# Optimization experiments

Hardware: AMD Instinct MI355X
Metric: run time of the kernel (lower is better)

Reference implementation:

```python
import jax, jax.numpy as jnp
import numpy as np

B, T, I, H, OUT, L = 256, 1200, 16, 128, 1, 2


def _lstm_layer(x, W_ih, W_hh, b_ih, b_hh):
    # x: [B, T, Din]; W_ih: [4H, Din]; W_hh: [4H, H]
    # Precompute input contribution for all timesteps (one big GEMM),
    # then scan only the recurrent part.
    pre = jnp.einsum('btd,gd->btg', x, W_ih) + b_ih + b_hh  # [B, T, 4H]
    pre = jnp.swapaxes(pre, 0, 1)  # [T, B, 4H]
    h0 = jnp.zeros((x.shape[0], W_hh.shape[1]), dtype=x.dtype)
    c0 = jnp.zeros_like(h0)

    def step(carry, p_t):
        h, c = carry
        g = p_t + h @ W_hh.T  # [B, 4H]
        i, f, gg, o = jnp.split(g, 4, axis=-1)  # torch gate order: i, f, g, o
        i = jax.nn.sigmoid(i)
        f = jax.nn.sigmoid(f)
        gg = jnp.tanh(gg)
        o = jax.nn.sigmoid(o)
        c = f * c + i * gg
        h = o * jnp.tanh(c)
        return (h, c), h

    (_, _), hs = jax.lax.scan(step, (h0, c0), pre)  # hs: [T, B, H]
    return jnp.swapaxes(hs, 0, 1)  # [B, T, H]


def setup_inputs() -> dict:
    key = jax.random.key(0)
    ks = jax.random.split(key, 12)
    s = 0.08  # small init scale to keep gates unsaturated
    inp = {
        'x': jax.random.normal(ks[0], (B, T, I), dtype=jnp.float32),
        'W_ih0': jax.random.normal(ks[1], (4 * H, I), dtype=jnp.float32) * s,
        'W_hh0': jax.random.normal(ks[2], (4 * H, H), dtype=jnp.float32) * s,
        'b_ih0': jax.random.normal(ks[3], (4 * H,), dtype=jnp.float32) * s,
        'b_hh0': jax.random.normal(ks[4], (4 * H,), dtype=jnp.float32) * s,
        'W_ih1': jax.random.normal(ks[5], (4 * H, H), dtype=jnp.float32) * s,
        'W_hh1': jax.random.normal(ks[6], (4 * H, H), dtype=jnp.float32) * s,
        'b_ih1': jax.random.normal(ks[7], (4 * H,), dtype=jnp.float32) * s,
        'b_hh1': jax.random.normal(ks[8], (4 * H,), dtype=jnp.float32) * s,
        'W_lin': jax.random.normal(ks[9], (OUT, H), dtype=jnp.float32) * s,
        'b_lin': jax.random.normal(ks[10], (OUT,), dtype=jnp.float32) * s,
    }
    return inp


def reference(x, W_ih0, W_hh0, b_ih0, b_hh0, W_ih1, W_hh1, b_ih1, b_hh1, W_lin, b_lin):
    h1 = _lstm_layer(x, W_ih0, W_hh0, b_ih0, b_hh0)   # [B, T, H]
    h2 = _lstm_layer(h1, W_ih1, W_hh1, b_ih1, b_hh1)  # [B, T, H]
    out = jax.nn.relu(h2)
    out = jnp.einsum('bth,oh->bto', out, W_lin) + b_lin  # [B, T, OUT]
    return out.reshape(-1, 12)  # [B*T*OUT/12, 12]
```

## Files before the change

### kernel.cpp

```cpp
#include <hip/hip_runtime.h>
#include <hip/hip_fp16.h>

#define B_ 256
#define T_ 1200
#define I_ 16
#define H_ 128
#define G4_ (4 * H_)

typedef __attribute__((ext_vector_type(2))) _Float16 h2;
typedef __attribute__((ext_vector_type(8))) _Float16 f16x8;

union f16x8u { f16x8 v; h2 h[4]; _Float16 s[8]; };

#if __has_builtin(__builtin_amdgcn_fdot2)
__device__ __forceinline__ float fdot2(h2 a, h2 b, float c) {
  return __builtin_amdgcn_fdot2(a, b, c, false);
}
#else
__device__ __forceinline__ float fdot2(h2 a, h2 b, float c) {
  return fmaf((float)a.x, (float)b.x, fmaf((float)a.y, (float)b.y, c));
}
#endif

template <int PAT>
__device__ __forceinline__ float qbcast(float x) {
  return __int_as_float(__builtin_amdgcn_update_dpp(0, __float_as_int(x), PAT, 0xF, 0xF, true));
}

__device__ __forceinline__ float wred(float x) {
  x += __int_as_float(__builtin_amdgcn_update_dpp(0, __float_as_int(x), 0x141, 0xF, 0xF, true));
  x += __int_as_float(__builtin_amdgcn_update_dpp(0, __float_as_int(x), 0x140, 0xF, 0xF, true));
  x += __shfl_xor(x, 16);
  x += __shfl_xor(x, 32);
  return x;
}

__device__ __forceinline__ float sigm(float x) {
  return __builtin_amdgcn_rcpf(1.f + __expf(-x));
}
__device__ __forceinline__ float tanh_(float x) {
  return 1.f - 2.f * __builtin_amdgcn_rcpf(1.f + __expf(2.f * x));
}

__device__ __forceinline__ void load_row_h2(const float* __restrict__ p, h2* w) {
#pragma unroll
  for (int i = 0; i < 32; ++i) {
    const float4 v = *(const float4*)(p + 4 * i);
    w[2 * i].x     = (_Float16)v.x; w[2 * i].y     = (_Float16)v.y;
    w[2 * i + 1].x = (_Float16)v.z; w[2 * i + 1].y = (_Float16)v.w;
  }
}

__global__ __launch_bounds__(512, 2) void k1_layer0(
    const float* __restrict__ xin,
    const float* __restrict__ Wih0, const float* __restrict__ Whh0,
    const float* __restrict__ bih0, const float* __restrict__ bhh0,
    __half* __restrict__ h0ws)
{
  __shared__ __align__(16) __half xs[T_ * I_];
  __shared__ __align__(16) __half hb[2][H_];

  const int tid = threadIdx.x;
  const int q = tid & 3;
  const int j = tid >> 2;
  const int g = q * H_ + j;
  const int b = blockIdx.x;

  {
    const float4* xg4 = (const float4*)(xin + (size_t)b * T_ * I_);
    for (int idx = tid; idx < T_ * I_ / 4; idx += 512) {
      const float4 v = xg4[idx];
      xs[4 * idx]     = __float2half(v.x);
      xs[4 * idx + 1] = __float2half(v.y);
      xs[4 * idx + 2] = __float2half(v.z);
      xs[4 * idx + 3] = __float2half(v.w);
    }
  }

  h2 wh[64], wx[8];
  load_row_h2(Whh0 + (size_t)g * H_, wh);
  {
    const float* px = Wih0 + (size_t)g * I_;
#pragma unroll
    for (int i = 0; i < 4; ++i) {
      const float4 v = *(const float4*)(px + 4 * i);
      wx[2 * i].x     = (_Float16)v.x; wx[2 * i].y     = (_Float16)v.y;
      wx[2 * i + 1].x = (_Float16)v.z; wx[2 * i + 1].y = (_Float16)v.w;
    }
  }
  const float bs = bih0[g] + bhh0[g];

  if (tid < H_) hb[0][tid] = __float2half(0.f);
  float cst = 0.f;
  __half* h0o = h0ws + (size_t)b * T_ * H_ + j;
  __syncthreads();

#pragma unroll 2
  for (int t = 0; t < T_; ++t) {
    const int rb = t & 1;
    float a0 = 0.f, a1 = 0.f, a2 = 0.f, a3 = 0.f;
#pragma unroll
    for (int i = 0; i < 16; ++i) {
      f16x8u u; u.v = *(const f16x8*)(&hb[rb][8 * i]);
      a0 = fdot2(wh[4 * i],     u.h[0], a0);
      a1 = fdot2(wh[4 * i + 1], u.h[1], a1);
      a2 = fdot2(wh[4 * i + 2], u.h[2], a2);
      a3 = fdot2(wh[4 * i + 3], u.h[3], a3);
    }
#pragma unroll
    for (int m = 0; m < 2; ++m) {
      f16x8u u; u.v = *(const f16x8*)(&xs[t * I_ + 8 * m]);
      a0 = fdot2(wx[4 * m],     u.h[0], a0);
      a1 = fdot2(wx[4 * m + 1], u.h[1], a1);
      a2 = fdot2(wx[4 * m + 2], u.h[2], a2);
      a3 = fdot2(wx[4 * m + 3], u.h[3], a3);
    }
    const float pre = (a0 + a1) + (a2 + a3) + bs;
    const float ip = qbcast<0x00>(pre);
    const float fp = qbcast<0x55>(pre);
    const float gp = qbcast<0xAA>(pre);
    const float op = qbcast<0xFF>(pre);
    const float ig = sigm(ip), fg = sigm(fp), gg = tanh_(gp), og = sigm(op);
    cst = fg * cst + ig * gg;
    const float hv = og * tanh_(cst);
    const __half hh = __float2half(hv);
    if (q == 0) {
      hb[rb ^ 1][j] = hh;
      h0o[(size_t)t * H_] = hh;
    }
    __syncthreads();
  }
}

__global__ __launch_bounds__(512, 2) void k2_pregemm(
    const __half* __restrict__ h0ws,
    const float* __restrict__ Wih1,
    __half* __restrict__ pre1)
{
  const int g = threadIdx.x;
  const int b = blockIdx.x;

  h2 w[64];
  load_row_h2(Wih1 + (size_t)g * H_, w);

  const __half* hrow = h0ws + (size_t)b * T_ * H_;
  __half* pp = pre1 + (size_t)b * T_ * G4_ + g;

#pragma unroll 2
  for (int t = 0; t < T_; ++t) {
    const __half* hr = hrow + (size_t)t * H_;
    float a0 = 0.f, a1 = 0.f, a2 = 0.f, a3 = 0.f;
#pragma unroll
    for (int i = 0; i < 16; ++i) {
      f16x8u u; u.v = *(const f16x8*)(hr + 8 * i);
      a0 = fdot2(w[4 * i],     u.h[0], a0);
      a1 = fdot2(w[4 * i + 1], u.h[1], a1);
      a2 = fdot2(w[4 * i + 2], u.h[2], a2);
      a3 = fdot2(w[4 * i + 3], u.h[3], a3);
    }
    pp[(size_t)t * G4_] = __float2half((a0 + a1) + (a2 + a3));
  }
}

__global__ __launch_bounds__(512, 2) void k3_layer1(
    const __half* __restrict__ pre1,
    const float* __restrict__ Whh1,
    const float* __restrict__ bih1, const float* __restrict__ bhh1,
    const float* __restrict__ Wlin, const float* __restrict__ blin,
    float* __restrict__ out)
{
  __shared__ __align__(16) __half hb[2][H_];
  __shared__ __align__(16) float red[2][8];

  const int tid = threadIdx.x;
  const int q = tid & 3;
  const int j = tid >> 2;
  const int g = q * H_ + j;
  const int b = blockIdx.x;
  const int wv = tid >> 6;

  h2 w[64];
  load_row_h2(Whh1 + (size_t)g * H_, w);
  const float bs = bih1[g] + bhh1[g];
  const float wl = Wlin[j];
  const float bl = blin[0];

  if (tid < H_) hb[0][tid] = __float2half(0.f);
  float cst = 0.f;
  const __half* pp = pre1 + (size_t)b * T_ * G4_ + g;
  float* op = out + (size_t)b * T_;
  __syncthreads();

  __half pnext = pp[0];
#pragma unroll 2
  for (int t = 0; t < T_; ++t) {
    const int rb = t & 1;
    const __half pcur = pnext;
    if (t + 1 < T_) pnext = pp[(size_t)(t + 1) * G4_];
    float a0 = 0.f, a1 = 0.f, a2 = 0.f, a3 = 0.f;
#pragma unroll
    for (int i = 0; i < 16; ++i) {
      f16x8u u; u.v = *(const f16x8*)(&hb[rb][8 * i]);
      a0 = fdot2(w[4 * i],     u.h[0], a0);
      a1 = fdot2(w[4 * i + 1], u.h[1], a1);
      a2 = fdot2(w[4 * i + 2], u.h[2], a2);
      a3 = fdot2(w[4 * i + 3], u.h[3], a3);
    }
    const float pre = (a0 + a1) + (a2 + a3) + __half2float(pcur) + bs;
    const float ip = qbcast<0x00>(pre);
    const float fp = qbcast<0x55>(pre);
    const float gp = qbcast<0xAA>(pre);
    const float op_ = qbcast<0xFF>(pre);
    const float ig = sigm(ip), fg = sigm(fp), gg = tanh_(gp), og = sigm(op_);
    cst = fg * cst + ig * gg;
    const float hv = og * tanh_(cst);
    if (q == 0) hb[rb ^ 1][j] = __float2half(hv);
    float val = wred(fmaxf(hv, 0.f) * wl);
    if ((tid & 63) == 0) red[rb][wv] = val;
    __syncthreads();
    if (tid == ((t & 7) << 6)) {
      const float4 r0 = *(const float4*)(&red[rb][0]);
      const float4 r1 = *(const float4*)(&red[rb][4]);
      op[t] = bl + r0.x + r0.y + r0.z + r0.w + r1.x + r1.y + r1.z + r1.w;
    }
  }
}

__device__ __forceinline__ float qsum8f(float x) {
  x += __int_as_float(__builtin_amdgcn_update_dpp(0, __float_as_int(x), 0xB1, 0xF, 0xF, true));
  x += __int_as_float(__builtin_amdgcn_update_dpp(0, __float_as_int(x), 0x4E, 0xF, 0xF, true));
  return x;
}

__global__ __launch_bounds__(512, 2) void lstm_fused_fb(
    const float* __restrict__ xin,
    const float* __restrict__ Wih0, const float* __restrict__ Whh0,
    const float* __restrict__ bih0, const float* __restrict__ bhh0,
    const float* __restrict__ Wih1, const float* __restrict__ Whh1,
    const float* __restrict__ bih1, const float* __restrict__ bhh1,
    const float* __restrict__ Wlin, const float* __restrict__ blin,
    float* __restrict__ out)
{
  __shared__ __align__(16) __half buf0[2][H_];
  __shared__ __align__(16) __half buf1[2][H_];
  __shared__ __align__(16) float red[2][8];

  const int tid = threadIdx.x;
  const int c = tid & 3;
  const int j = tid >> 2;
  const int b = blockIdx.x;
  const int wv = tid >> 6;

  h2 w0[4][16], wi[4][16], wh[4][16];
  h2 wx[4][2];
  float bs0[4], bs1[4];

#pragma unroll
  for (int qq = 0; qq < 4; ++qq) {
    const int g = qq * H_ + j;
    const float* p0 = Whh0 + (size_t)g * H_ + c * 32;
    const float* p1 = Wih1 + (size_t)g * H_ + c * 32;
    const float* p2 = Whh1 + (size_t)g * H_ + c * 32;
#pragma unroll
    for (int i = 0; i < 8; ++i) {
      float4 v = *(const float4*)(p0 + 4 * i);
      w0[qq][2*i].x   = (_Float16)v.x; w0[qq][2*i].y   = (_Float16)v.y;
      w0[qq][2*i+1].x = (_Float16)v.z; w0[qq][2*i+1].y = (_Float16)v.w;
      v = *(const float4*)(p1 + 4 * i);
      wi[qq][2*i].x   = (_Float16)v.x; wi[qq][2*i].y   = (_Float16)v.y;
      wi[qq][2*i+1].x = (_Float16)v.z; wi[qq][2*i+1].y = (_Float16)v.w;
      v = *(const float4*)(p2 + 4 * i);
      wh[qq][2*i].x   = (_Float16)v.x; wh[qq][2*i].y   = (_Float16)v.y;
      wh[qq][2*i+1].x = (_Float16)v.z; wh[qq][2*i+1].y = (_Float16)v.w;
    }
    const float4 vx = *(const float4*)(Wih0 + (size_t)g * I_ + 4 * c);
    wx[qq][0].x = (_Float16)vx.x; wx[qq][0].y = (_Float16)vx.y;
    wx[qq][1].x = (_Float16)vx.z; wx[qq][1].y = (_Float16)vx.w;
    bs0[qq] = bih0[g] + bhh0[g];
    bs1[qq] = bih1[g] + bhh1[g];
  }
  const float wl = Wlin[j];
  const float bl = blin[0];

  if (tid < H_) {
    buf0[0][tid] = __float2half(0.f);
    buf1[0][tid] = __float2half(0.f);
  }
  float cst0 = 0.f, cst1 = 0.f;
  const float* xp = xin + (size_t)b * T_ * I_ + 4 * c;
  float* op = out + (size_t)b * T_;
  __syncthreads();

#pragma unroll 2
  for (int t = 0; t < T_; ++t) {
    const int rb = t & 1;
    const float4 xv = *(const float4*)xp; xp += I_;
    float a0 = 0.f, a1 = 0.f, a2 = 0.f, a3 = 0.f;
#pragma unroll
    for (int i = 0; i < 4; ++i) {
      f16x8u u; u.v = *(const f16x8*)(&buf0[rb][c * 32 + i * 8]);
#pragma unroll
      for (int p = 0; p < 4; ++p) {
        const h2 hv = u.h[p];
        a0 = fdot2(w0[0][4 * i + p], hv, a0);
        a1 = fdot2(w0[1][4 * i + p], hv, a1);
        a2 = fdot2(w0[2][4 * i + p], hv, a2);
        a3 = fdot2(w0[3][4 * i + p], hv, a3);
      }
    }
    h2 xa, xb;
    xa.x = (_Float16)xv.x; xa.y = (_Float16)xv.y;
    xb.x = (_Float16)xv.z; xb.y = (_Float16)xv.w;
    a0 = fdot2(wx[0][0], xa, fdot2(wx[0][1], xb, a0));
    a1 = fdot2(wx[1][0], xa, fdot2(wx[1][1], xb, a1));
    a2 = fdot2(wx[2][0], xa, fdot2(wx[2][1], xb, a2));
    a3 = fdot2(wx[3][0], xa, fdot2(wx[3][1], xb, a3));
    {
      const float g0 = qsum8f(a0) + bs0[0];
      const float g1 = qsum8f(a1) + bs0[1];
      const float g2 = qsum8f(a2) + bs0[2];
      const float g3 = qsum8f(a3) + bs0[3];
      const float ig = sigm(g0), fg = sigm(g1), gg = tanh_(g2), og = sigm(g3);
      cst0 = fg * cst0 + ig * gg;
      const float h0v = og * tanh_(cst0);
      if (c == 0) buf0[rb ^ 1][j] = __float2half(h0v);
    }
    __syncthreads();
    a0 = 0.f; a1 = 0.f; a2 = 0.f; a3 = 0.f;
#pragma unroll
    for (int i = 0; i < 4; ++i) {
      f16x8u u; u.v = *(const f16x8*)(&buf0[rb ^ 1][c * 32 + i * 8]);
#pragma unroll
      for (int p = 0; p < 4; ++p) {
        const h2 hv = u.h[p];
        a0 = fdot2(wi[0][4 * i + p], hv, a0);
        a1 = fdot2(wi[1][4 * i + p], hv, a1);
        a2 = fdot2(wi[2][4 * i + p], hv, a2);
        a3 = fdot2(wi[3][4 * i + p], hv, a3);
      }
    }
#pragma unroll
    for (int i = 0; i < 4; ++i) {
      f16x8u u; u.v = *(const f16x8*)(&buf1[rb][c * 32 + i * 8]);
#pragma unroll
      for (int p = 0; p < 4; ++p) {
        const h2 hv = u.h[p];
        a0 = fdot2(wh[0][4 * i + p], hv, a0);
        a1 = fdot2(wh[1][4 * i + p], hv, a1);
        a2 = fdot2(wh[2][4 * i + p], hv, a2);
        a3 = fdot2(wh[3][4 * i + p], hv, a3);
      }
    }
    const float g0 = qsum8f(a0) + bs1[0];
    const float g1 = qsum8f(a1) + bs1[1];
    const float g2 = qsum8f(a2) + bs1[2];
    const float g3 = qsum8f(a3) + bs1[3];
    const float ig = sigm(g0), fg = sigm(g1), gg = tanh_(g2), og = sigm(g3);
    cst1 = fg * cst1 + ig * gg;
    const float h1v = og * tanh_(cst1);
    if (c == 0) buf1[rb ^ 1][j] = __float2half(h1v);
    float val = wred(fmaxf(h1v, 0.f) * wl);
    if ((tid & 63) == 0) red[rb][wv] = val;
    __syncthreads();
    if (tid == ((t & 7) << 6)) {
      const float4 r0 = *(const float4*)(&red[rb][0]);
      const float4 r1 = *(const float4*)(&red[rb][4]);
      op[t] = bl + r0.x + r0.y + r0.z + r0.w + r1.x + r1.y + r1.z + r1.w;
    }
  }
}

extern "C" void kernel_launch(void* const* d_in, const int* in_sizes, int n_in,
                              void* d_out, int out_size, void* d_ws, size_t ws_size,
                              hipStream_t stream) {
  const size_t H0_BYTES  = (size_t)B_ * T_ * H_ * sizeof(__half);
  const size_t PRE_BYTES = (size_t)B_ * T_ * G4_ * sizeof(__half);

  if (d_ws != nullptr && ws_size >= H0_BYTES + PRE_BYTES) {
    __half* h0ws = (__half*)d_ws;
    __half* pre1 = (__half*)((char*)d_ws + H0_BYTES);
    k1_layer0<<<B_, 512, 0, stream>>>(
        (const float*)d_in[0],
        (const float*)d_in[1], (const float*)d_in[2],
        (const float*)d_in[3], (const float*)d_in[4],
        h0ws);
    k2_pregemm<<<B_, 512, 0, stream>>>(
        h0ws, (const float*)d_in[5], pre1);
    k3_layer1<<<B_, 512, 0, stream>>>(
        pre1, (const float*)d_in[6],
        (const float*)d_in[7], (const float*)d_in[8],
        (const float*)d_in[9], (const float*)d_in[10],
        (float*)d_out);
  } else {
    lstm_fused_fb<<<B_, 512, 0, stream>>>(
        (const float*)d_in[0],
        (const float*)d_in[1], (const float*)d_in[2],
        (const float*)d_in[3], (const float*)d_in[4],
        (const float*)d_in[5], (const float*)d_in[6],
        (const float*)d_in[7], (const float*)d_in[8],
        (const float*)d_in[9], (const float*)d_in[10],
        (float*)d_out);
  }
}
```

Before: 1.751 ms.

## Fuse layer-1 input GEMM into recurrent kernel with producer/consumer warps

Result: slower. 1.927 ms (+10.0%).

```diff
diff --git a/kernel.cpp b/kernel.cpp
--- a/kernel.cpp
+++ b/kernel.cpp
@@ -5,7 +5,7 @@
 #define T_ 1200
 #define I_ 16
 #define H_ 128
-#define G4_ (4 * H_)
+#define NT_ (T_ / 8)
 
 typedef __attribute__((ext_vector_type(2))) _Float16 h2;
 typedef __attribute__((ext_vector_type(8))) _Float16 f16x8;
@@ -89,6 +89,9 @@
     }
   }
   const float bs = bih0[g] + bhh0[g];
+  const float s0 = (q == 2) ? 1.f : 0.f;
+  const float s1 = (q == 2) ? -2.f : 1.f;
+  const float s2 = (q == 2) ? 2.f : -1.f;
 
   if (tid < H_) hb[0][tid] = __float2half(0.f);
   float cst = 0.f;
@@ -116,11 +119,11 @@
       a3 = fdot2(wx[4 * m + 3], u.h[3], a3);
     }
     const float pre = (a0 + a1) + (a2 + a3) + bs;
-    const float ip = qbcast<0x00>(pre);
-    const float fp = qbcast<0x55>(pre);
-    const float gp = qbcast<0xAA>(pre);
-    const float op = qbcast<0xFF>(pre);
-    const float ig = sigm(ip), fg = sigm(fp), gg = tanh_(gp), og = sigm(op);
+    const float act = fmaf(s1, __builtin_amdgcn_rcpf(1.f + __expf(s2 * pre)), s0);
+    const float ig = qbcast<0x00>(act);
+    const float fg = qbcast<0x55>(act);
+    const float gg = qbcast<0xAA>(act);
+    const float og = qbcast<0xFF>(act);
     cst = fg * cst + ig * gg;
     const float hv = og * tanh_(cst);
     const __half hh = __float2half(hv);
@@ -132,97 +135,118 @@
   }
 }
 
-__global__ __launch_bounds__(512, 2) void k2_pregemm(
+__global__ __attribute__((amdgpu_waves_per_eu(4, 4)))
+__launch_bounds__(1024) void kb_layer1(
     const __half* __restrict__ h0ws,
-    const float* __restrict__ Wih1,
-    __half* __restrict__ pre1)
+    const float* __restrict__ Wih1, const float* __restrict__ Whh1,
+    const float* __restrict__ bih1, const float* __restrict__ bhh1,
+    const float* __restrict__ Wlin, const float* __restrict__ blin,
+    float* __restrict__ out)
 {
-  const int g = threadIdx.x;
+  __shared__ __align__(16) __half h0til[2][8 * H_];
+  __shared__ __align__(16) float aih[2][512];
+  __shared__ __align__(16) __half h1b[2][H_];
+  __shared__ __align__(16) float red[2][8];
+
+  const int tid = threadIdx.x;
+  const bool isA = tid < 512;
+  const int lid = tid & 511;
+  const int q = lid & 3;
+  const int j = lid >> 2;
+  const int g = q * H_ + j;
   const int b = blockIdx.x;
 
   h2 w[64];
-  load_row_h2(Wih1 + (size_t)g * H_, w);
-
-  const __half* hrow = h0ws + (size_t)b * T_ * H_;
-  __half* pp = pre1 + (size_t)b * T_ * G4_ + g;
-
-#pragma unroll 2
-  for (int t = 0; t < T_; ++t) {
-    const __half* hr = hrow + (size_t)t * H_;
+  load_row_h2((isA ? Wih1 : Whh1) + (size_t)g * H_, w);
+
+  const float bs = bih1[g] + bhh1[g];
+  const float wl = Wlin[j];
+  const float bl = blin[0];
+  const float s0 = (q == 2) ? 1.f : 0.f;
+  const float s1 = (q == 2) ? -2.f : 1.f;
+  const float s2 = (q == 2) ? 2.f : -1.f;
+
+  const uint* h0u = (const uint*)(h0ws + (size_t)b * T_ * H_);
+
+  if (isA) ((uint*)h0til[0])[lid] = h0u[lid];
+  if (!isA && lid < H_) h1b[0][lid] = __float2half(0.f);
+  __syncthreads();
+  if (isA) {
     float a0 = 0.f, a1 = 0.f, a2 = 0.f, a3 = 0.f;
 #pragma unroll
     for (int i = 0; i < 16; ++i) {
-      f16x8u u; u.v = *(const f16x8*)(hr + 8 * i);
+      f16x8u u; u.v = *(const f16x8*)(&h0til[0][8 * i]);
       a0 = fdot2(w[4 * i],     u.h[0], a0);
       a1 = fdot2(w[4 * i + 1], u.h[1], a1);
       a2 = fdot2(w[4 * i + 2], u.h[2], a2);
       a3 = fdot2(w[4 * i + 3], u.h[3], a3);
     }
-    pp[(size_t)t * G4_] = __float2half((a0 + a1) + (a2 + a3));
-  }
-}
-
-__global__ __launch_bounds__(512, 2) void k3_layer1(
-    const __half* __restrict__ pre1,
-    const float* __restrict__ Whh1,
-    const float* __restrict__ bih1, const float* __restrict__ bhh1,
-    const float* __restrict__ Wlin, const float* __restrict__ blin,
-    float* __restrict__ out)
-{
-  __shared__ __align__(16) __half hb[2][H_];
-  __shared__ __align__(16) float red[2][8];
-
-  const int tid = threadIdx.x;
-  const int q = tid & 3;
-  const int j = tid >> 2;
-  const int g = q * H_ + j;
-  const int b = blockIdx.x;
-  const int wv = tid >> 6;
-
-  h2 w[64];
-  load_row_h2(Whh1 + (size_t)g * H_, w);
-  const float bs = bih1[g] + bhh1[g];
-  const float wl = Wlin[j];
-  const float bl = blin[0];
-
-  if (tid < H_) hb[0][tid] = __float2half(0.f);
+    aih[0][lid] = (a0 + a1) + (a2 + a3);
+  }
+  __syncthreads();
+
   float cst = 0.f;
-  const __half* pp = pre1 + (size_t)b * T_ * G4_ + g;
+  uint stg = 0;
   float* op = out + (size_t)b * T_;
-  __syncthreads();
-
-  __half pnext = pp[0];
-#pragma unroll 2
+
   for (int t = 0; t < T_; ++t) {
     const int rb = t & 1;
-    const __half pcur = pnext;
-    if (t + 1 < T_) pnext = pp[(size_t)(t + 1) * G4_];
-    float a0 = 0.f, a1 = 0.f, a2 = 0.f, a3 = 0.f;
-#pragma unroll
-    for (int i = 0; i < 16; ++i) {
-      f16x8u u; u.v = *(const f16x8*)(&hb[rb][8 * i]);
-      a0 = fdot2(w[4 * i],     u.h[0], a0);
-      a1 = fdot2(w[4 * i + 1], u.h[1], a1);
-      a2 = fdot2(w[4 * i + 2], u.h[2], a2);
-      a3 = fdot2(w[4 * i + 3], u.h[3], a3);
-    }
-    const float pre = (a0 + a1) + (a2 + a3) + __half2float(pcur) + bs;
-    const float ip = qbcast<0x00>(pre);
-    const float fp = qbcast<0x55>(pre);
-    const float gp = qbcast<0xAA>(pre);
-    const float op_ = qbcast<0xFF>(pre);
-    const float ig = sigm(ip), fg = sigm(fp), gg = tanh_(gp), og = sigm(op_);
-    cst = fg * cst + ig * gg;
-    const float hv = og * tanh_(cst);
-    if (q == 0) hb[rb ^ 1][j] = __float2half(hv);
-    float val = wred(fmaxf(hv, 0.f) * wl);
-    if ((tid & 63) == 0) red[rb][wv] = val;
+    if (isA) {
+      if ((t & 7) == 0) {
+        const int m1 = (t >> 3) + 1;
+        if (m1 < NT_) stg = h0u[m1 * 512 + lid];
+      }
+      const int tt = t + 1;
+      if (tt < T_) {
+        const __half* hsrc = &h0til[(tt >> 3) & 1][(tt & 7) * H_];
+        float a0 = 0.f, a1 = 0.f, a2 = 0.f, a3 = 0.f;
+#pragma unroll
+        for (int i = 0; i < 16; ++i) {
+          f16x8u u; u.v = *(const f16x8*)(hsrc + 8 * i);
+          a0 = fdot2(w[4 * i],     u.h[0], a0);
+          a1 = fdot2(w[4 * i + 1], u.h[1], a1);
+          a2 = fdot2(w[4 * i + 2], u.h[2], a2);
+          a3 = fdot2(w[4 * i + 3], u.h[3], a3);
+        }
+        aih[tt & 1][lid] = (a0 + a1) + (a2 + a3);
+      }
+      if ((t & 7) == 6) {
+        const int m1 = (t >> 3) + 1;
+        if (m1 < NT_) ((uint*)h0til[m1 & 1])[lid] = stg;
+      }
+    } else {
+      float a0 = 0.f, a1 = 0.f, a2 = 0.f, a3 = 0.f;
+#pragma unroll
+      for (int i = 0; i < 16; ++i) {
+        f16x8u u; u.v = *(const f16x8*)(&h1b[rb][8 * i]);
+        a0 = fdot2(w[4 * i],     u.h[0], a0);
+        a1 = fdot2(w[4 * i + 1], u.h[1], a1);
+        a2 = fdot2(w[4 * i + 2], u.h[2], a2);
+        a3 = fdot2(w[4 * i + 3], u.h[3], a3);
+      }
+      const float pre = (a0 + a1) + (a2 + a3) + aih[rb][lid] + bs;
+      const float act = fmaf(s1, __builtin_amdgcn_rcpf(1.f + __expf(s2 * pre)), s0);
+      const float ig = qbcast<0x00>(act);
+      const float fg = qbcast<0x55>(act);
+      const float gg = qbcast<0xAA>(act);
+      const float og = qbcast<0xFF>(act);
+      cst = fg * cst + ig * gg;
+      const float hv = og * tanh_(cst);
+      if (q == 0) h1b[rb ^ 1][j] = __float2half(hv);
+      const float val = wred(fmaxf(hv, 0.f) * wl);
+      if ((lid & 63) == 0) red[rb][lid >> 6] = val;
+      if (t > 0 && lid == (((t - 1) & 7) << 6)) {
+        const float4 r0 = *(const float4*)(&red[rb ^ 1][0]);
+        const float4 r1 = *(const float4*)(&red[rb ^ 1][4]);
+        op[t - 1] = bl + r0.x + r0.y + r0.z + r0.w + r1.x + r1.y + r1.z + r1.w;
+      }
+    }
     __syncthreads();
-    if (tid == ((t & 7) << 6)) {
-      const float4 r0 = *(const float4*)(&red[rb][0]);
-      const float4 r1 = *(const float4*)(&red[rb][4]);
-      op[t] = bl + r0.x + r0.y + r0.z + r0.w + r1.x + r1.y + r1.z + r1.w;
-    }
+  }
+  if (!isA && lid == (((T_ - 1) & 7) << 6)) {
+    const float4 r0 = *(const float4*)(&red[(T_ - 1) & 1][0]);
+    const float4 r1 = *(const float4*)(&red[(T_ - 1) & 1][4]);
+    op[T_ - 1] = bl + r0.x + r0.y + r0.z + r0.w + r1.x + r1.y + r1.z + r1.w;
   }
 }
 
@@ -373,21 +397,18 @@
 extern "C" void kernel_launch(void* const* d_in, const int* in_sizes, int n_in,
                               void* d_out, int out_size, void* d_ws, size_t ws_size,
                               hipStream_t stream) {
-  const size_t H0_BYTES  = (size_t)B_ * T_ * H_ * sizeof(__half);
-  const size_t PRE_BYTES = (size_t)B_ * T_ * G4_ * sizeof(__half);
-
-  if (d_ws != nullptr && ws_size >= H0_BYTES + PRE_BYTES) {
+  const size_t H0_BYTES = (size_t)B_ * T_ * H_ * sizeof(__half);
+
+  if (d_ws != nullptr && ws_size >= H0_BYTES) {
     __half* h0ws = (__half*)d_ws;
-    __half* pre1 = (__half*)((char*)d_ws + H0_BYTES);
     k1_layer0<<<B_, 512, 0, stream>>>(
         (const float*)d_in[0],
         (const float*)d_in[1], (const float*)d_in[2],
         (const float*)d_in[3], (const float*)d_in[4],
         h0ws);
-    k2_pregemm<<<B_, 512, 0, stream>>>(
-        h0ws, (const float*)d_in[5], pre1);
-    k3_layer1<<<B_, 512, 0, stream>>>(
-        pre1, (const float*)d_in[6],
+    kb_layer1<<<B_, 1024, 0, stream>>>(
+        h0ws,
+        (const float*)d_in[5], (const float*)d_in[6],
         (const float*)d_in[7], (const float*)d_in[8],
         (const float*)d_in[9], (const float*)d_in[10],
         (float*)d_out);
```
